# Kernel tuning notes

Measured on AMD Instinct MI355X. Metric: run time of the kernel, lower is better.

Reference implementation:

```python
import jax, jax.numpy as jnp
import numpy as np

N_HEADS = 8
WINDOW = 64
NEG = -1e9


def _layer_norm(x, g, b, eps=1e-5):
    mu = jnp.mean(x, axis=-1, keepdims=True)
    var = jnp.mean((x - mu) ** 2, axis=-1, keepdims=True)
    return g * (x - mu) / jnp.sqrt(var + eps) + b


def _sinusoidal_pe(S, D):
    pos = jnp.arange(S, dtype=jnp.float32)[:, None]
    div = jnp.exp(jnp.arange(0, D, 2, dtype=jnp.float32) * (-jnp.log(jnp.float32(10000.0)) / D))
    pe = jnp.zeros((S, D), jnp.float32)
    pe = pe.at[:, 0::2].set(jnp.sin(pos * div))
    pe = pe.at[:, 1::2].set(jnp.cos(pos * div))
    return pe


def setup_inputs():
    key = jax.random.key(0)
    ks = jax.random.split(key, 8)
    L, S, D, DFF = 4, 2048, 1024, 2048
    p = lambda k, shape: jax.random.normal(k, shape, jnp.float32) * 0.02
    return {
        "T": 1800,
        "enc_inputs": jax.random.normal(ks[0], (1, S, D), jnp.float32),
        "global_idx": jax.random.randint(ks[1], (32,), 0, 27000),
        "Wq": p(ks[2], (L, D, D)),
        "Wk": p(ks[3], (L, D, D)),
        "Wv": p(ks[4], (L, D, D)),
        "Wo": p(ks[5], (L, D, D)),
        "ln1_g": jnp.ones((L, D), jnp.float32),
        "ln1_b": jnp.zeros((L, D), jnp.float32),
        "W1": p(ks[6], (L, D, DFF)),
        "W2": p(ks[7], (L, DFF, D)),
        "ln2_g": jnp.ones((L, D), jnp.float32),
        "ln2_b": jnp.zeros((L, D), jnp.float32),
    }


def reference(T, enc_inputs, global_idx, Wq, Wk, Wv, Wo, ln1_g, ln1_b, W1, W2, ln2_g, ln2_b):
    B, S, D = enc_inputs.shape
    L = Wq.shape[0]
    H, DK = N_HEADS, D // N_HEADS

    # enc_outputs = enc_inputs + PE(enc_inputs) = 2*enc_inputs + pe (faithful to source)
    pe = _sinusoidal_pe(S, D)
    x = enc_inputs + (enc_inputs + pe[None])

    # mask vector: 1 = local token, -1 = global token, 0 = pad
    idx = jnp.arange(S)
    mvec = jnp.where(idx < T, 1.0, 0.0)
    g = global_idx // 15
    valid = (g >= 0) & (g < S)
    is_global = jnp.any((idx[None, :] == g[:, None]) & valid[:, None], axis=0)
    mvec = jnp.where(is_global, jnp.float32(-1.0), mvec)

    half = WINDOW // 2
    local = jnp.abs(idx[:, None] - idx[None, :]) <= half
    nonpad = mvec != 0.0
    glob = mvec == -1.0
    allowed = nonpad[:, None] & nonpad[None, :] & (local | glob[:, None] | glob[None, :])
    scale = 1.0 / jnp.sqrt(jnp.float32(DK))

    for l in range(L):
        # local-global multi-head self-attention
        q = (x @ Wq[l]).reshape(B, S, H, DK).transpose(0, 2, 1, 3)
        k = (x @ Wk[l]).reshape(B, S, H, DK).transpose(0, 2, 1, 3)
        v = (x @ Wv[l]).reshape(B, S, H, DK).transpose(0, 2, 1, 3)
        scores = jnp.einsum("bhqd,bhkd->bhqk", q, k) * scale
        scores = jnp.where(allowed[None, None], scores, jnp.float32(NEG))
        attn = jax.nn.softmax(scores, axis=-1)
        ctx = jnp.einsum("bhqk,bhkd->bhqd", attn, v).transpose(0, 2, 1, 3).reshape(B, S, D)
        x = _layer_norm(ctx @ Wo[l] + x, ln1_g[l], ln1_b[l])
        # position-wise FFN with residual + LayerNorm
        h = jax.nn.relu(x @ W1[l]) @ W2[l]
        x = _layer_norm(h + x, ln2_g[l], ln2_b[l])

    return x[0]  # squeeze(0): (S, D)
```

## Files before the change

kernel.cpp:

```cpp
#include <hip/hip_runtime.h>
#include <cstdint>
#include <cstddef>

#define S_LEN  2048
#define D_MODEL 1024
#define D_FF   2048
#define NLAYER 4

typedef float  f32x4  __attribute__((ext_vector_type(4)));
typedef __bf16 bf16x8 __attribute__((ext_vector_type(8)));
typedef __bf16 bf16x4 __attribute__((ext_vector_type(4)));

#define ATT_SCALE 0.08838834764831845f

__device__ __forceinline__ void async_copy16(const void* g, void* s) {
    __builtin_amdgcn_global_load_lds((const __attribute__((address_space(1))) void*)g,
                                     (__attribute__((address_space(3))) void*)s, 16, 0, 0);
}

template<int NW>
__device__ __forceinline__ float blockRedSum(float v, float* red) {
    #pragma unroll
    for (int off = 32; off > 0; off >>= 1) v += __shfl_down(v, off);
    const int t = threadIdx.x;
    if ((t & 63) == 0) red[t >> 6] = v;
    __syncthreads();
    float r = red[0];
    #pragma unroll
    for (int i = 1; i < NW; i++) r += red[i];
    __syncthreads();
    return r;
}

__global__ __launch_bounds__(256)
void init_mask_kernel(const float* __restrict__ enc, float* __restrict__ x,
                      __bf16* __restrict__ xb, const int* __restrict__ gidx,
                      int* __restrict__ isg, int* __restrict__ gcols, int* __restrict__ ngc,
                      float* __restrict__ vmean) {
    const int t = threadIdx.x;
    if (blockIdx.x < S_LEN) {
        const int s = blockIdx.x;
        #pragma unroll
        for (int i = 0; i < 4; i++) {
            const int d = t + i * 256;
            const float freq = expf(-(float)(d & ~1) * (9.210340371976184f / 1024.0f));
            const float ang = (float)s * freq;
            const float pe = (d & 1) ? cosf(ang) : sinf(ang);
            const float v = 2.0f * enc[(size_t)s * D_MODEL + d] + pe;
            x[(size_t)s * D_MODEL + d] = v;
            xb[(size_t)s * D_MODEL + d] = (__bf16)v;
        }
    } else {
        #pragma unroll
        for (int i = 0; i < 4; i++) vmean[t + i * 256] = 0.0f;
        __shared__ int gsh[32];
        __shared__ int cnt;
        if (t < 32) {
            const int g = gidx[t] / 15;
            gsh[t] = (g >= 0 && g < S_LEN) ? g : -1;
        }
        if (t == 0) cnt = 0;
        __syncthreads();
        #pragma unroll
        for (int i = 0; i < 8; i++) {
            const int s = t + i * 256;
            int f = 0;
            #pragma unroll
            for (int j = 0; j < 32; j++) f |= (gsh[j] == s) ? 1 : 0;
            isg[s] = f;
            if (f) { const int p = atomicAdd(&cnt, 1); gcols[p] = s; }
        }
        __syncthreads();
        if (t == 0) *ngc = cnt;
    }
}

__global__ __launch_bounds__(256)
void transpose_all_kernel(const float* __restrict__ Wq, const float* __restrict__ Wk,
                          const float* __restrict__ Wv, const float* __restrict__ Wo,
                          const float* __restrict__ W1, const float* __restrict__ W2,
                          __bf16* __restrict__ out) {
    const int layer = blockIdx.x >> 9;
    const int r = blockIdx.x & 511;
    const size_t lw = (size_t)layer * 1024 * 1024;
    const size_t lf = (size_t)layer * 1024 * 2048;
    __bf16* arena = out + (size_t)layer * 8 * 1024 * 1024;
    const float* in; __bf16* o; int K, N, n0, k0;
    if (r < 256) {
        const int m = r >> 6, rr = r & 63;
        in = ((m == 0) ? Wq : (m == 1) ? Wk : (m == 2) ? Wv : Wo) + lw;
        o  = arena + (size_t)m * 1024 * 1024;
        K = 1024; N = 1024; n0 = (rr & 7) * 128; k0 = (rr >> 3) * 128;
    } else if (r < 384) {
        const int rr = r - 256;
        in = W1 + lf; o = arena + (size_t)4 * 1024 * 1024;
        K = 1024; N = 2048; n0 = (rr & 15) * 128; k0 = (rr >> 4) * 128;
    } else {
        const int rr = r - 384;
        in = W2 + lf; o = arena + (size_t)6 * 1024 * 1024;
        K = 2048; N = 1024; n0 = (rr & 7) * 128; k0 = (rr >> 3) * 128;
    }
    __shared__ __bf16 tile[128][148];
    const int t = threadIdx.x;
    {
        const int tx = t & 127, tp = t >> 7;
        #pragma unroll
        for (int j2 = tp; j2 < 64; j2 += 2) {
            const float a = in[(size_t)(k0 + 2 * j2)     * N + n0 + tx];
            const float b = in[(size_t)(k0 + 2 * j2 + 1) * N + n0 + tx];
            __bf16 pr[2] = {(__bf16)a, (__bf16)b};
            *(uint32_t*)&tile[tx][2 * j2] = *(uint32_t*)pr;
        }
    }
    __syncthreads();
    {
        const int ktx = t & 31, j0 = t >> 5;
        #pragma unroll
        for (int j = j0; j < 128; j += 8) {
            const bf16x4 v = *(const bf16x4*)&tile[j][4 * ktx];
            *(bf16x4*)&o[(size_t)(n0 + j) * K + k0 + 4 * ktx] = v;
        }
    }
}

template<int BM, int BN, int EPI, bool VACC>
__global__ __launch_bounds__(256)
void gemm_bt(const __bf16* __restrict__ A, const __bf16* __restrict__ Bt,
             void* __restrict__ Cv, float* __restrict__ vmean, int M, int N, int K) {
    constexpr int WM = BM / 2, WN = BN / 2;
    constexpr int MI = WM / 16, NI = WN / 16;
    constexpr int RA = BM / 32, RB = BN / 32;
    __shared__ __bf16 As[BM * 64];
    __shared__ __bf16 Bs[BN * 64];
    const int t = threadIdx.x;
    const int w = t >> 6, l = t & 63;
    const int l15 = l & 15, q4 = l >> 4;
    const int wr = w >> 1, wc = w & 1;
    const int m0 = blockIdx.y * BM, n0 = blockIdx.x * BN;

    const int srow = t >> 3;
    const int kc8  = (((t & 7) ^ (srow & 7)) * 8);
    const __bf16* ag = A  + (size_t)(m0 + srow) * K + kc8;
    const __bf16* bg = Bt + (size_t)(n0 + srow) * K + kc8;
    __bf16* asw = As + w * 512;
    __bf16* bsw = Bs + w * 512;

    const int r7 = l15 & 7;
    int arow[MI], brow[NI];
    #pragma unroll
    for (int i = 0; i < MI; i++) arow[i] = (wr * WM + i * 16 + l15) * 64;
    #pragma unroll
    for (int j = 0; j < NI; j++) brow[j] = (wc * WN + j * 16 + l15) * 64;

    f32x4 acc[MI][NI];
    #pragma unroll
    for (int i = 0; i < MI; i++)
        #pragma unroll
        for (int j = 0; j < NI; j++) acc[i][j] = (f32x4){0.f, 0.f, 0.f, 0.f};

    for (int k0 = 0; k0 < K; k0 += 64) {
        #pragma unroll
        for (int rr = 0; rr < RA; rr++)
            async_copy16(ag + (size_t)rr * 32 * K + k0, asw + rr * 2048);
        #pragma unroll
        for (int rr = 0; rr < RB; rr++)
            async_copy16(bg + (size_t)rr * 32 * K + k0, bsw + rr * 2048);
        __syncthreads();
        #pragma unroll
        for (int s = 0; s < 64; s += 32) {
            const int slot = ((q4 + (s >> 3)) ^ r7) * 8;
            bf16x8 af[MI], bfr[NI];
            #pragma unroll
            for (int i = 0; i < MI; i++) af[i]  = *(const bf16x8*)(As + arow[i] + slot);
            #pragma unroll
            for (int j = 0; j < NI; j++) bfr[j] = *(const bf16x8*)(Bs + brow[j] + slot);
            #pragma unroll
            for (int i = 0; i < MI; i++)
                #pragma unroll
                for (int j = 0; j < NI; j++)
                    acc[i][j] = __builtin_amdgcn_mfma_f32_16x16x32_bf16(af[i], bfr[j], acc[i][j], 0, 0, 0);
        }
        __syncthreads();
    }

    const int r0 = m0 + wr * WM + q4 * 4;
    const int c0 = n0 + wc * WN + l15;
    if constexpr (EPI == 0) {
        float* C = (float*)Cv;
        #pragma unroll
        for (int i = 0; i < MI; i++)
            #pragma unroll
            for (int j = 0; j < NI; j++)
                #pragma unroll
                for (int r = 0; r < 4; r++)
                    C[(size_t)(r0 + i * 16 + r) * N + c0 + j * 16] = acc[i][j][r];
    } else if constexpr (EPI == 1) {
        __bf16* C = (__bf16*)Cv;
        #pragma unroll
        for (int i = 0; i < MI; i++)
            #pragma unroll
            for (int j = 0; j < NI; j++)
                #pragma unroll
                for (int r = 0; r < 4; r++)
                    C[(size_t)(r0 + i * 16 + r) * N + c0 + j * 16] = (__bf16)fmaxf(acc[i][j][r], 0.0f);
    } else {
        __bf16* C = (__bf16*)Cv;
        #pragma unroll
        for (int i = 0; i < MI; i++)
            #pragma unroll
            for (int j = 0; j < NI; j++)
                #pragma unroll
                for (int r = 0; r < 4; r++)
                    C[(size_t)(r0 + i * 16 + r) * N + c0 + j * 16] = (__bf16)acc[i][j][r];
    }
    if constexpr (VACC) {
        #pragma unroll
        for (int j = 0; j < NI; j++) {
            const int col = c0 + j * 16;
            if (col >= 2048) {
                float s = 0.f;
                #pragma unroll
                for (int i = 0; i < MI; i++)
                    #pragma unroll
                    for (int r = 0; r < 4; r++) s += acc[i][j][r];
                s += __shfl_xor(s, 16);
                s += __shfl_xor(s, 32);
                if (q4 == 0) atomicAdd(&vmean[col - 2048], s);
            }
        }
    }
}

__global__ __launch_bounds__(256)
void attn_kernel(const __bf16* __restrict__ qkvb, const int* __restrict__ Tp,
                 const int* __restrict__ isg, const int* __restrict__ gcols,
                 const int* __restrict__ ngcp, const float* __restrict__ vmean,
                 __bf16* __restrict__ ctx, float* __restrict__ Og,
                 float* __restrict__ mg, float* __restrict__ lg) {
    const int h = blockIdx.y, hd = h * 128;
    const int t = threadIdx.x;
    const int T = *Tp, ng = *ngcp;
    __shared__ __bf16 Qs[32 * 136];
    __shared__ __bf16 Ks[128 * 136];
    __shared__ __bf16 Vs[128 * 136];
    __shared__ __bf16 Ps[32 * 136];
    __shared__ float  Ss[32 * 129];
    __shared__ int cix[128], cgf[128], rtype[32];
    __shared__ int ncs;
    const int l = t & 63, w = t >> 6;
    const int l15 = l & 15, q4 = l >> 4;
    const int nb = w * 32;

    if (blockIdx.x < 64) {
        const int qt0 = blockIdx.x * 32;
        const int wl = max(qt0 - 32, 0), wh = min(qt0 + 63, S_LEN - 1);
        if (t == 0) ncs = 0;
        if (t < 32) { const int qr = qt0 + t; rtype[t] = isg[qr] ? 1 : (qr < T ? 0 : 2); }
        __syncthreads();
        if (t <= wh - wl) {
            const int c = wl + t, gf = isg[c];
            if (c < T || gf) { const int p = atomicAdd(&ncs, 1); cix[p] = c; cgf[p] = gf; }
        }
        if (t < ng) {
            const int c = gcols[t];
            if (c < wl || c > wh) { const int p = atomicAdd(&ncs, 1); cix[p] = c; cgf[p] = 1; }
        }
        {
            const int r = t >> 3, d0 = (t & 7) * 16;
            const bf16x8* src = (const bf16x8*)(qkvb + (size_t)(qt0 + r) * 3072 + hd + d0);
            *(bf16x8*)&Qs[r * 136 + d0]     = src[0];
            *(bf16x8*)&Qs[r * 136 + d0 + 8] = src[1];
        }
        __syncthreads();
        const int nc = ncs;
        if (nc + t < 128) { cix[nc + t] = -1; cgf[nc + t] = 0; }
        {
            const int j = t >> 1, d0 = (t & 1) * 64;
            const int ci = (j < nc) ? cix[j] : -1;
            if (ci >= 0) {
                const bf16x8* kp = (const bf16x8*)(qkvb + (size_t)ci * 3072 + 1024 + hd + d0);
                const bf16x8* vp = (const bf16x8*)(qkvb + (size_t)ci * 3072 + 2048 + hd + d0);
                #pragma unroll
                for (int i = 0; i < 8; i++) {
                    *(bf16x8*)&Ks[j * 136 + d0 + i * 8] = kp[i];
                    *(bf16x8*)&Vs[j * 136 + d0 + i * 8] = vp[i];
                }
            } else {
                #pragma unroll
                for (int i = 0; i < 8; i++) {
                    *(bf16x8*)&Ks[j * 136 + d0 + i * 8] = (bf16x8)(__bf16)0.f;
                    *(bf16x8*)&Vs[j * 136 + d0 + i * 8] = (bf16x8)(__bf16)0.f;
                }
            }
        }
        __syncthreads();
        {
            f32x4 sacc[2][2];
            #pragma unroll
            for (int i = 0; i < 2; i++)
                #pragma unroll
                for (int j = 0; j < 2; j++) sacc[i][j] = (f32x4){0.f, 0.f, 0.f, 0.f};
            #pragma unroll
            for (int kk = 0; kk < 4; kk++) {
                const int k0 = kk * 32;
                bf16x8 af[2], bk[2];
                af[0] = *(const bf16x8*)&Qs[l15 * 136 + k0 + q4 * 8];
                af[1] = *(const bf16x8*)&Qs[(16 + l15) * 136 + k0 + q4 * 8];
                bk[0] = *(const bf16x8*)&Ks[(nb + l15) * 136 + k0 + q4 * 8];
                bk[1] = *(const bf16x8*)&Ks[(nb + 16 + l15) * 136 + k0 + q4 * 8];
                #pragma unroll
                for (int m2 = 0; m2 < 2; m2++)
                    #pragma unroll
                    for (int n2 = 0; n2 < 2; n2++)
                        sacc[m2][n2] = __builtin_amdgcn_mfma_f32_16x16x32_bf16(af[m2], bk[n2], sacc[m2][n2], 0, 0, 0);
            }
            #pragma unroll
            for (int m2 = 0; m2 < 2; m2++)
                #pragma unroll
                for (int n2 = 0; n2 < 2; n2++)
                    #pragma unroll
                    for (int r = 0; r < 4; r++) {
                        const int row = m2 * 16 + q4 * 4 + r;
                        const int col = nb + n2 * 16 + l15;
                        const int c = cix[col];
                        const int dd = qt0 + row - c;
                        const bool ok = (c >= 0) && (((unsigned)(dd + 32) <= 64u) || cgf[col]);
                        Ss[row * 129 + col] = ok ? sacc[m2][n2][r] * ATT_SCALE : -1e30f;
                    }
        }
        __syncthreads();
        {
            const int r = t >> 3, i = t & 7;
            float mx = -1e30f;
            for (int c = i; c < 128; c += 8) mx = fmaxf(mx, Ss[r * 129 + c]);
            #pragma unroll
            for (int off = 4; off > 0; off >>= 1) mx = fmaxf(mx, __shfl_down(mx, off, 8));
            mx = __shfl(mx, 0, 8);
            float sm = 0.f;
            for (int c = i; c < 128; c += 8) {
                const float s = Ss[r * 129 + c];
                const float p = (s > -1e29f) ? __expf(s - mx) : 0.f;
                Ss[r * 129 + c] = p;
                sm += p;
            }
            #pragma unroll
            for (int off = 4; off > 0; off >>= 1) sm += __shfl_down(sm, off, 8);
            sm = __shfl(sm, 0, 8);
            const float rl = 1.0f / fmaxf(sm, 1e-30f);
            for (int c = i; c < 128; c += 8) Ps[r * 136 + c] = (__bf16)(Ss[r * 129 + c] * rl);
        }
        __syncthreads();
        {
            f32x4 oacc[2][2];
            #pragma unroll
            for (int i = 0; i < 2; i++)
                #pragma unroll
                for (int j = 0; j < 2; j++) oacc[i][j] = (f32x4){0.f, 0.f, 0.f, 0.f};
            #pragma unroll
            for (int kk = 0; kk < 4; kk++) {
                const int k0 = kk * 32;
                bf16x8 ap[2], bv[2];
                ap[0] = *(const bf16x8*)&Ps[l15 * 136 + k0 + q4 * 8];
                ap[1] = *(const bf16x8*)&Ps[(16 + l15) * 136 + k0 + q4 * 8];
                #pragma unroll
                for (int n2 = 0; n2 < 2; n2++) {
                    const int dimn = nb + n2 * 16 + l15;
                    #pragma unroll
                    for (int jj = 0; jj < 8; jj++)
                        bv[n2][jj] = Vs[(k0 + q4 * 8 + jj) * 136 + dimn];
                }
                #pragma unroll
                for (int m2 = 0; m2 < 2; m2++)
                    #pragma unroll
                    for (int n2 = 0; n2 < 2; n2++)
                        oacc[m2][n2] = __builtin_amdgcn_mfma_f32_16x16x32_bf16(ap[m2], bv[n2], oacc[m2][n2], 0, 0, 0);
            }
            #pragma unroll
            for (int m2 = 0; m2 < 2; m2++)
                #pragma unroll
                for (int n2 = 0; n2 < 2; n2++)
                    #pragma unroll
                    for (int r = 0; r < 4; r++) {
                        const int row = m2 * 16 + q4 * 4 + r;
                        const int dim = nb + n2 * 16 + l15;
                        const int rt = rtype[row];
                        const size_t o = (size_t)(qt0 + row) * D_MODEL + hd + dim;
                        if (rt == 0)      ctx[o] = (__bf16)oacc[m2][n2][r];
                        else if (rt == 2) ctx[o] = (__bf16)(vmean[hd + dim] * (1.0f / 2048.0f));
                    }
        }
    } else {
        if (ng == 0) return;
        const int cb = blockIdx.x - 64, c0 = cb * 128;
        {
            const int r = t >> 3, d0 = (t & 7) * 16;
            if (r < ng) {
                const bf16x8* src = (const bf16x8*)(qkvb + (size_t)gcols[r] * 3072 + hd + d0);
                *(bf16x8*)&Qs[r * 136 + d0]     = src[0];
                *(bf16x8*)&Qs[r * 136 + d0 + 8] = src[1];
            } else {
                *(bf16x8*)&Qs[r * 136 + d0]     = (bf16x8)(__bf16)0.f;
                *(bf16x8*)&Qs[r * 136 + d0 + 8] = (bf16x8)(__bf16)0.f;
            }
        }
        if (t < 128) { const int c = c0 + t; cix[t] = (c < T || isg[c]) ? 1 : 0; }
        {
            const int j = t >> 1, d0 = (t & 1) * 64;
            const int ci = c0 + j;
            const bf16x8* kp = (const bf16x8*)(qkvb + (size_t)ci * 3072 + 1024 + hd + d0);
            const bf16x8* vp = (const bf16x8*)(qkvb + (size_t)ci * 3072 + 2048 + hd + d0);
            #pragma unroll
            for (int i = 0; i < 8; i++) {
                *(bf16x8*)&Ks[j * 136 + d0 + i * 8] = kp[i];
                *(bf16x8*)&Vs[j * 136 + d0 + i * 8] = vp[i];
            }
        }
        __syncthreads();
        {
            f32x4 sacc[2][2];
            #pragma unroll
            for (int i = 0; i < 2; i++)
                #pragma unroll
                for (int j = 0; j < 2; j++) sacc[i][j] = (f32x4){0.f, 0.f, 0.f, 0.f};
            #pragma unroll
            for (int kk = 0; kk < 4; kk++) {
                const int k0 = kk * 32;
                bf16x8 af[2], bk[2];
                af[0] = *(const bf16x8*)&Qs[l15 * 136 + k0 + q4 * 8];
                af[1] = *(const bf16x8*)&Qs[(16 + l15) * 136 + k0 + q4 * 8];
                bk[0] = *(const bf16x8*)&Ks[(nb + l15) * 136 + k0 + q4 * 8];
                bk[1] = *(const bf16x8*)&Ks[(nb + 16 + l15) * 136 + k0 + q4 * 8];
                #pragma unroll
                for (int m2 = 0; m2 < 2; m2++)
                    #pragma unroll
                    for (int n2 = 0; n2 < 2; n2++)
                        sacc[m2][n2] = __builtin_amdgcn_mfma_f32_16x16x32_bf16(af[m2], bk[n2], sacc[m2][n2], 0, 0, 0);
            }
            #pragma unroll
            for (int m2 = 0; m2 < 2; m2++)
                #pragma unroll
                for (int n2 = 0; n2 < 2; n2++)
                    #pragma unroll
                    for (int r = 0; r < 4; r++) {
                        const int row = m2 * 16 + q4 * 4 + r;
                        const int col = nb + n2 * 16 + l15;
                        Ss[row * 129 + col] = cix[col] ? sacc[m2][n2][r] * ATT_SCALE : -1e30f;
                    }
        }
        __syncthreads();
        {
            const int r = t >> 3, i = t & 7;
            float mx = -1e30f;
            for (int c = i; c < 128; c += 8) mx = fmaxf(mx, Ss[r * 129 + c]);
            #pragma unroll
            for (int off = 4; off > 0; off >>= 1) mx = fmaxf(mx, __shfl_down(mx, off, 8));
            mx = __shfl(mx, 0, 8);
            float sm = 0.f;
            for (int c = i; c < 128; c += 8) {
                const float s = Ss[r * 129 + c];
                const float p = (s > -1e29f) ? __expf(s - mx) : 0.f;
                Ps[r * 136 + c] = (__bf16)p;
                sm += p;
            }
            #pragma unroll
            for (int off = 4; off > 0; off >>= 1) sm += __shfl_down(sm, off, 8);
            if (i == 0) { mg[(h * 16 + cb) * 32 + r] = mx; lg[(h * 16 + cb) * 32 + r] = sm; }
        }
        __syncthreads();
        {
            f32x4 oacc[2][2];
            #pragma unroll
            for (int i = 0; i < 2; i++)
                #pragma unroll
                for (int j = 0; j < 2; j++) oacc[i][j] = (f32x4){0.f, 0.f, 0.f, 0.f};
            #pragma unroll
            for (int kk = 0; kk < 4; kk++) {
                const int k0 = kk * 32;
                bf16x8 ap[2], bv[2];
                ap[0] = *(const bf16x8*)&Ps[l15 * 136 + k0 + q4 * 8];
                ap[1] = *(const bf16x8*)&Ps[(16 + l15) * 136 + k0 + q4 * 8];
                #pragma unroll
                for (int n2 = 0; n2 < 2; n2++) {
                    const int dimn = nb + n2 * 16 + l15;
                    #pragma unroll
                    for (int jj = 0; jj < 8; jj++)
                        bv[n2][jj] = Vs[(k0 + q4 * 8 + jj) * 136 + dimn];
                }
                #pragma unroll
                for (int m2 = 0; m2 < 2; m2++)
                    #pragma unroll
                    for (int n2 = 0; n2 < 2; n2++)
                        oacc[m2][n2] = __builtin_amdgcn_mfma_f32_16x16x32_bf16(ap[m2], bv[n2], oacc[m2][n2], 0, 0, 0);
            }
            #pragma unroll
            for (int m2 = 0; m2 < 2; m2++)
                #pragma unroll
                for (int n2 = 0; n2 < 2; n2++)
                    #pragma unroll
                    for (int r = 0; r < 4; r++) {
                        const int row = m2 * 16 + q4 * 4 + r;
                        const int dim = nb + n2 * 16 + l15;
                        Og[((size_t)(h * 16 + cb) * 32 + row) * 128 + dim] = oacc[m2][n2][r];
                    }
        }
    }
}

__global__ __launch_bounds__(256)
void attn_gcomb(const int* __restrict__ gcols, const int* __restrict__ ngcp,
                const float* __restrict__ Og, const float* __restrict__ mg,
                const float* __restrict__ lg, __bf16* __restrict__ ctx) {
    const int h = blockIdx.x, hd = h * 128, t = threadIdx.x;
    const int ng = *ngcp;
    const int r = t >> 3, i = t & 7;
    if (r >= ng) return;
    float M = -1e30f;
    #pragma unroll
    for (int cb = 0; cb < 16; cb++) M = fmaxf(M, mg[(h * 16 + cb) * 32 + r]);
    float e[16], L = 0.f;
    #pragma unroll
    for (int cb = 0; cb < 16; cb++) {
        e[cb] = __expf(mg[(h * 16 + cb) * 32 + r] - M);
        L += e[cb] * lg[(h * 16 + cb) * 32 + r];
    }
    const float rL = 1.0f / fmaxf(L, 1e-30f);
    const int grow = gcols[r];
    for (int d = i; d < 128; d += 8) {
        float o = 0.f;
        #pragma unroll
        for (int cb = 0; cb < 16; cb++)
            o += e[cb] * Og[((size_t)(h * 16 + cb) * 32 + r) * 128 + d];
        ctx[(size_t)grow * D_MODEL + hd + d] = (__bf16)(o * rL);
    }
}

__global__ __launch_bounds__(256)
void ln_kernel(const float* __restrict__ y, const float* __restrict__ r,
               const float* __restrict__ g, const float* __restrict__ b,
               float* __restrict__ xo, __bf16* __restrict__ xb, float* __restrict__ vz) {
    const int row = blockIdx.x, t = threadIdx.x;
    if (vz != nullptr && row == 0) {
        #pragma unroll
        for (int i = 0; i < 4; i++) vz[t + i * 256] = 0.0f;
    }
    const float* yr = y + (size_t)row * D_MODEL;
    const float* rr = r + (size_t)row * D_MODEL;
    __shared__ float red[4];
    float v[4]; float s = 0.f;
    #pragma unroll
    for (int i = 0; i < 4; i++) { const int d = t + i * 256; v[i] = yr[d] + rr[d]; s += v[i]; }
    s = blockRedSum<4>(s, red);
    const float mu = s * (1.0f / 1024.0f);
    float vs = 0.f;
    #pragma unroll
    for (int i = 0; i < 4; i++) { const float dd = v[i] - mu; vs += dd * dd; }
    vs = blockRedSum<4>(vs, red);
    const float rstd = rsqrtf(vs * (1.0f / 1024.0f) + 1e-5f);
    #pragma unroll
    for (int i = 0; i < 4; i++) {
        const int d = t + i * 256;
        const float o = g[d] * (v[i] - mu) * rstd + b[d];
        xo[(size_t)row * D_MODEL + d] = o;
        xb[(size_t)row * D_MODEL + d] = (__bf16)o;
    }
}

extern "C" void kernel_launch(void* const* d_in, const int* in_sizes, int n_in,
                              void* d_out, int out_size, void* d_ws, size_t ws_size,
                              hipStream_t stream) {
    const int*   Tp   = (const int*)  d_in[0];
    const float* enc  = (const float*)d_in[1];
    const int*   gidx = (const int*)  d_in[2];
    const float* Wq   = (const float*)d_in[3];
    const float* Wk   = (const float*)d_in[4];
    const float* Wv   = (const float*)d_in[5];
    const float* Wo   = (const float*)d_in[6];
    const float* ln1g = (const float*)d_in[7];
    const float* ln1b = (const float*)d_in[8];
    const float* W1   = (const float*)d_in[9];
    const float* W2   = (const float*)d_in[10];
    const float* ln2g = (const float*)d_in[11];
    const float* ln2b = (const float*)d_in[12];

    char* p = (char*)d_ws;
    size_t off = 0;
    auto alloc = [&](size_t bytes) -> void* {
        void* q = p + off;
        off += (bytes + 255) & ~(size_t)255;
        return q;
    };
    float*  x     = (float*) alloc((size_t)S_LEN * D_MODEL * 4);
    __bf16* xb    = (__bf16*)alloc((size_t)S_LEN * D_MODEL * 2);
    __bf16* qkvb  = (__bf16*)alloc((size_t)S_LEN * 3072 * 2);
    __bf16* ctx   = (__bf16*)alloc((size_t)S_LEN * D_MODEL * 2);
    float*  g1    = (float*) alloc((size_t)S_LEN * D_MODEL * 4);
    __bf16* h1    = (__bf16*)alloc((size_t)S_LEN * D_FF * 2);
    __bf16* wT    = (__bf16*)alloc((size_t)4 * 8 * 1024 * 1024 * 2);
    float*  vmean = (float*) alloc(1024 * 4);
    int*    isg   = (int*)   alloc(S_LEN * 4);
    int*    gcols = (int*)   alloc(S_LEN * 4);
    int*    ngc   = (int*)   alloc(256);
    float*  Og    = (float*) alloc((size_t)8 * 16 * 32 * 128 * 4);
    float*  mgb   = (float*) alloc(8 * 16 * 32 * 4);
    float*  lgb   = (float*) alloc(8 * 16 * 32 * 4);

    init_mask_kernel<<<S_LEN + 1, 256, 0, stream>>>(enc, x, xb, gidx, isg, gcols, ngc, vmean);
    transpose_all_kernel<<<2048, 256, 0, stream>>>(Wq, Wk, Wv, Wo, W1, W2, wT);

    for (int l = 0; l < NLAYER; l++) {
        __bf16* wL = wT + (size_t)l * 8 * 1024 * 1024;
        gemm_bt<64, 128, 2, true><<<dim3(24, 32), 256, 0, stream>>>(xb, wL, (void*)qkvb, vmean, S_LEN, 3072, 1024);

        attn_kernel<<<dim3(80, 8), 256, 0, stream>>>(qkvb, Tp, isg, gcols, ngc, vmean, ctx, Og, mgb, lgb);
        attn_gcomb<<<8, 256, 0, stream>>>(gcols, ngc, Og, mgb, lgb, ctx);

        gemm_bt<64, 64, 0, false><<<dim3(16, 32), 256, 0, stream>>>(ctx, wL + (size_t)3 * 1024 * 1024, (void*)g1, nullptr, S_LEN, 1024, 1024);
        ln_kernel<<<S_LEN, 256, 0, stream>>>(g1, x, ln1g + l * 1024, ln1b + l * 1024, x, xb, nullptr);

        gemm_bt<64, 64, 1, false><<<dim3(32, 32), 256, 0, stream>>>(xb, wL + (size_t)4 * 1024 * 1024, (void*)h1, nullptr, S_LEN, 2048, 1024);
        gemm_bt<64, 64, 0, false><<<dim3(16, 32), 256, 0, stream>>>(h1, wL + (size_t)6 * 1024 * 1024, (void*)g1, nullptr, S_LEN, 1024, 2048);
        float* xout = (l == NLAYER - 1) ? (float*)d_out : x;
        ln_kernel<<<S_LEN, 256, 0, stream>>>(g1, x, ln2g + l * 1024, ln2b + l * 1024, xout, xb, vmean);
    }
}
```

Baseline: 682.8 us.

## Fuse global-row combine into attention via last-block atomic counter; shrink transpose tiles

Removes the separate attn_gcomb launch by having the last of the 16 global-column blocks per head, found through an atomic counter, perform the softmax-merge of the partial outputs, with thread fences for visibility. Per-layer counters are zeroed in the init kernel. The weight transpose kernel also switches to 64-wide N tiles with twice as many blocks and a smaller shared tile. This saves a launch per layer and gives the transpose more parallelism, at the cost of added fence and atomic overhead and a serial tail on the last block.

New measurement: 737.5 us. 8.0% more time.

```diff
diff --git a/kernel.cpp b/kernel.cpp
--- a/kernel.cpp
+++ b/kernel.cpp
@@ -36,7 +36,7 @@
 void init_mask_kernel(const float* __restrict__ enc, float* __restrict__ x,
                       __bf16* __restrict__ xb, const int* __restrict__ gidx,
                       int* __restrict__ isg, int* __restrict__ gcols, int* __restrict__ ngc,
-                      float* __restrict__ vmean) {
+                      float* __restrict__ vmean, int* __restrict__ gcnt) {
     const int t = threadIdx.x;
     if (blockIdx.x < S_LEN) {
         const int s = blockIdx.x;
@@ -53,6 +53,7 @@
     } else {
         #pragma unroll
         for (int i = 0; i < 4; i++) vmean[t + i * 256] = 0.0f;
+        if (t < 32) gcnt[t] = 0;
         __shared__ int gsh[32];
         __shared__ int cnt;
         if (t < 32) {
@@ -80,43 +81,43 @@
                           const float* __restrict__ Wv, const float* __restrict__ Wo,
                           const float* __restrict__ W1, const float* __restrict__ W2,
                           __bf16* __restrict__ out) {
-    const int layer = blockIdx.x >> 9;
-    const int r = blockIdx.x & 511;
+    const int layer = blockIdx.x >> 10;
+    const int r = blockIdx.x & 1023;
     const size_t lw = (size_t)layer * 1024 * 1024;
     const size_t lf = (size_t)layer * 1024 * 2048;
     __bf16* arena = out + (size_t)layer * 8 * 1024 * 1024;
     const float* in; __bf16* o; int K, N, n0, k0;
-    if (r < 256) {
-        const int m = r >> 6, rr = r & 63;
+    if (r < 512) {
+        const int m = r >> 7, rr = r & 127;
         in = ((m == 0) ? Wq : (m == 1) ? Wk : (m == 2) ? Wv : Wo) + lw;
         o  = arena + (size_t)m * 1024 * 1024;
-        K = 1024; N = 1024; n0 = (rr & 7) * 128; k0 = (rr >> 3) * 128;
-    } else if (r < 384) {
-        const int rr = r - 256;
+        K = 1024; N = 1024; n0 = (rr & 15) * 64; k0 = (rr >> 4) * 128;
+    } else if (r < 768) {
+        const int rr = r - 512;
         in = W1 + lf; o = arena + (size_t)4 * 1024 * 1024;
-        K = 1024; N = 2048; n0 = (rr & 15) * 128; k0 = (rr >> 4) * 128;
+        K = 1024; N = 2048; n0 = (rr & 31) * 64; k0 = (rr >> 5) * 128;
     } else {
-        const int rr = r - 384;
+        const int rr = r - 768;
         in = W2 + lf; o = arena + (size_t)6 * 1024 * 1024;
-        K = 2048; N = 1024; n0 = (rr & 7) * 128; k0 = (rr >> 3) * 128;
-    }
-    __shared__ __bf16 tile[128][148];
+        K = 2048; N = 1024; n0 = (rr & 15) * 64; k0 = (rr >> 4) * 128;
+    }
+    __shared__ __bf16 tile[64][130];
     const int t = threadIdx.x;
     {
-        const int tx = t & 127, tp = t >> 7;
-        #pragma unroll
-        for (int j2 = tp; j2 < 64; j2 += 2) {
-            const float a = in[(size_t)(k0 + 2 * j2)     * N + n0 + tx];
-            const float b = in[(size_t)(k0 + 2 * j2 + 1) * N + n0 + tx];
+        const int nx = t & 63, tp = t >> 6;
+        #pragma unroll
+        for (int j2 = tp; j2 < 64; j2 += 4) {
+            const float a = in[(size_t)(k0 + 2 * j2)     * N + n0 + nx];
+            const float b = in[(size_t)(k0 + 2 * j2 + 1) * N + n0 + nx];
             __bf16 pr[2] = {(__bf16)a, (__bf16)b};
-            *(uint32_t*)&tile[tx][2 * j2] = *(uint32_t*)pr;
+            *(uint32_t*)&tile[nx][2 * j2] = *(uint32_t*)pr;
         }
     }
     __syncthreads();
     {
         const int ktx = t & 31, j0 = t >> 5;
         #pragma unroll
-        for (int j = j0; j < 128; j += 8) {
+        for (int j = j0; j < 64; j += 8) {
             const bf16x4 v = *(const bf16x4*)&tile[j][4 * ktx];
             *(bf16x4*)&o[(size_t)(n0 + j) * K + k0 + 4 * ktx] = v;
         }
@@ -236,7 +237,8 @@
                  const int* __restrict__ isg, const int* __restrict__ gcols,
                  const int* __restrict__ ngcp, const float* __restrict__ vmean,
                  __bf16* __restrict__ ctx, float* __restrict__ Og,
-                 float* __restrict__ mg, float* __restrict__ lg) {
+                 float* __restrict__ mg, float* __restrict__ lg,
+                 int* __restrict__ gcnt, int layer) {
     const int h = blockIdx.y, hd = h * 128;
     const int t = threadIdx.x;
     const int T = *Tp, ng = *ngcp;
@@ -503,34 +505,32 @@
                         Og[((size_t)(h * 16 + cb) * 32 + row) * 128 + dim] = oacc[m2][n2][r];
                     }
         }
-    }
-}
-
-__global__ __launch_bounds__(256)
-void attn_gcomb(const int* __restrict__ gcols, const int* __restrict__ ngcp,
-                const float* __restrict__ Og, const float* __restrict__ mg,
-                const float* __restrict__ lg, __bf16* __restrict__ ctx) {
-    const int h = blockIdx.x, hd = h * 128, t = threadIdx.x;
-    const int ng = *ngcp;
-    const int r = t >> 3, i = t & 7;
-    if (r >= ng) return;
-    float M = -1e30f;
-    #pragma unroll
-    for (int cb = 0; cb < 16; cb++) M = fmaxf(M, mg[(h * 16 + cb) * 32 + r]);
-    float e[16], L = 0.f;
-    #pragma unroll
-    for (int cb = 0; cb < 16; cb++) {
-        e[cb] = __expf(mg[(h * 16 + cb) * 32 + r] - M);
-        L += e[cb] * lg[(h * 16 + cb) * 32 + r];
-    }
-    const float rL = 1.0f / fmaxf(L, 1e-30f);
-    const int grow = gcols[r];
-    for (int d = i; d < 128; d += 8) {
-        float o = 0.f;
-        #pragma unroll
-        for (int cb = 0; cb < 16; cb++)
-            o += e[cb] * Og[((size_t)(h * 16 + cb) * 32 + r) * 128 + d];
-        ctx[(size_t)grow * D_MODEL + hd + d] = (__bf16)(o * rL);
+        __threadfence();
+        __syncthreads();
+        if (t == 0) ncs = (atomicAdd(&gcnt[layer * 8 + h], 1) == 15) ? 1 : 0;
+        __syncthreads();
+        if (!ncs) return;
+        __threadfence();
+        const int r = t >> 3, i = t & 7;
+        if (r >= ng) return;
+        float M = -1e30f;
+        #pragma unroll
+        for (int cb2 = 0; cb2 < 16; cb2++) M = fmaxf(M, mg[(h * 16 + cb2) * 32 + r]);
+        float e[16], L = 0.f;
+        #pragma unroll
+        for (int cb2 = 0; cb2 < 16; cb2++) {
+            e[cb2] = __expf(mg[(h * 16 + cb2) * 32 + r] - M);
+            L += e[cb2] * lg[(h * 16 + cb2) * 32 + r];
+        }
+        const float rL = 1.0f / fmaxf(L, 1e-30f);
+        const int grow = gcols[r];
+        for (int d = i; d < 128; d += 8) {
+            float o = 0.f;
+            #pragma unroll
+            for (int cb2 = 0; cb2 < 16; cb2++)
+                o += e[cb2] * Og[((size_t)(h * 16 + cb2) * 32 + r) * 128 + d];
+            ctx[(size_t)grow * D_MODEL + hd + d] = (__bf16)(o * rL);
+        }
     }
 }
 
@@ -603,16 +603,16 @@
     float*  Og    = (float*) alloc((size_t)8 * 16 * 32 * 128 * 4);
     float*  mgb   = (float*) alloc(8 * 16 * 32 * 4);
     float*  lgb   = (float*) alloc(8 * 16 * 32 * 4);
-
-    init_mask_kernel<<<S_LEN + 1, 256, 0, stream>>>(enc, x, xb, gidx, isg, gcols, ngc, vmean);
-    transpose_all_kernel<<<2048, 256, 0, stream>>>(Wq, Wk, Wv, Wo, W1, W2, wT);
+    int*    gcnt  = (int*)   alloc(32 * 4);
+
+    init_mask_kernel<<<S_LEN + 1, 256, 0, stream>>>(enc, x, xb, gidx, isg, gcols, ngc, vmean, gcnt);
+    transpose_all_kernel<<<4096, 256, 0, stream>>>(Wq, Wk, Wv, Wo, W1, W2, wT);
 
     for (int l = 0; l < NLAYER; l++) {
         __bf16* wL = wT + (size_t)l * 8 * 1024 * 1024;
         gemm_bt<64, 128, 2, true><<<dim3(24, 32), 256, 0, stream>>>(xb, wL, (void*)qkvb, vmean, S_LEN, 3072, 1024);
 
-        attn_kernel<<<dim3(80, 8), 256, 0, stream>>>(qkvb, Tp, isg, gcols, ngc, vmean, ctx, Og, mgb, lgb);
-        attn_gcomb<<<8, 256, 0, stream>>>(gcols, ngc, Og, mgb, lgb, ctx);
+        attn_kernel<<<dim3(80, 8), 256, 0, stream>>>(qkvb, Tp, isg, gcols, ngc, vmean, ctx, Og, mgb, lgb, gcnt, l);
 
         gemm_bt<64, 64, 0, false><<<dim3(16, 32), 256, 0, stream>>>(ctx, wL + (size_t)3 * 1024 * 1024, (void*)g1, nullptr, S_LEN, 1024, 1024);
         ln_kernel<<<S_LEN, 256, 0, stream>>>(g1, x, ln1g + l * 1024, ln1b + l * 1024, x, xb, nullptr);
```
